# Kernel tuning notes

Hardware: AMD Instinct MI355X
Metric: run time of the kernel (lower is better)

## Reference

```python
import jax, jax.numpy as jnp
import numpy as np

DIM = 256
NH = 8
PD = DIM // 16  # DynamicPosBias pos_dim = (dim//4)//4 = 16
B_ = 256
GH = 16
GW = 16
N = GH * GW
NG = 64


def setup_inputs() -> dict:
    key = jax.random.key(0)
    ks = jax.random.split(key, 24)
    s = 0.05
    inp = {
        "q": jax.random.normal(ks[0], (B_, N, DIM), dtype=jnp.float32),
        "k": jax.random.normal(ks[1], (B_, N, DIM), dtype=jnp.float32),
        "mask": jax.random.normal(ks[2], (NG, N, N), dtype=jnp.float32),
        "q_w": jax.random.normal(ks[3], (DIM, DIM), dtype=jnp.float32) * s,
        "q_b": jnp.zeros((DIM,), jnp.float32),
        "kv_w": jax.random.normal(ks[4], (2 * DIM, DIM), dtype=jnp.float32) * s,
        "kv_b": jnp.zeros((2 * DIM,), jnp.float32),
        "proj_w": jax.random.normal(ks[5], (DIM, DIM), dtype=jnp.float32) * s,
        "proj_b": jnp.zeros((DIM,), jnp.float32),
        "pp_w": jax.random.normal(ks[6], (PD, 2), dtype=jnp.float32) * s,
        "pp_b": jnp.zeros((PD,), jnp.float32),
        "ln1_g": jnp.ones((PD,), jnp.float32),
        "ln1_b": jnp.zeros((PD,), jnp.float32),
        "l1_w": jax.random.normal(ks[7], (PD, PD), dtype=jnp.float32) * s,
        "l1_b": jnp.zeros((PD,), jnp.float32),
        "ln2_g": jnp.ones((PD,), jnp.float32),
        "ln2_b": jnp.zeros((PD,), jnp.float32),
        "l2_w": jax.random.normal(ks[8], (PD, PD), dtype=jnp.float32) * s,
        "l2_b": jnp.zeros((PD,), jnp.float32),
        "ln3_g": jnp.ones((PD,), jnp.float32),
        "ln3_b": jnp.zeros((PD,), jnp.float32),
        "l3_w": jax.random.normal(ks[9], (NH, PD), dtype=jnp.float32) * s,
        "l3_b": jnp.zeros((NH,), jnp.float32),
        "H": GH,
        "W": GW,
    }
    return inp


def _ln(x, g, b):
    m = x.mean(-1, keepdims=True)
    v = ((x - m) ** 2).mean(-1, keepdims=True)
    return (x - m) / jnp.sqrt(v + 1e-5) * g + b


def _pos_bias(H, W, pp_w, pp_b, ln1_g, ln1_b, l1_w, l1_b, ln2_g, ln2_b, l2_w, l2_b, ln3_g, ln3_b, l3_w, l3_b):
    # biases: ((2H-1)*(2W-1), 2) relative offsets
    bh = jnp.arange(1 - H, H, dtype=jnp.float32)
    bw = jnp.arange(1 - W, W, dtype=jnp.float32)
    mg = jnp.stack(jnp.meshgrid(bh, bw, indexing="ij"))  # (2, 2H-1, 2W-1)
    biases = mg.reshape(2, -1).T  # (L, 2)
    # MLP (residual=False): pos3(pos2(pos1(pos_proj(b))))
    x = biases @ pp_w.T + pp_b
    x = _ln(x, ln1_g, ln1_b)
    x = jax.nn.relu(x) @ l1_w.T + l1_b
    x = _ln(x, ln2_g, ln2_b)
    x = jax.nn.relu(x) @ l2_w.T + l2_b
    x = _ln(x, ln3_g, ln3_b)
    pos = jax.nn.relu(x) @ l3_w.T + l3_b  # (L, NH)
    # relative position index (N, N)
    ch = jnp.arange(H)
    cw = jnp.arange(W)
    coords = jnp.stack(jnp.meshgrid(ch, cw, indexing="ij")).reshape(2, -1)  # (2, N)
    rel = coords[:, :, None] - coords[:, None, :]  # (2, N, N)
    rel = rel.transpose(1, 2, 0)
    rel = rel + jnp.array([H - 1, W - 1])
    idx = rel[..., 0] * (2 * W - 1) + rel[..., 1]  # (N, N)
    rpb = pos[idx.reshape(-1)].reshape(H * W, H * W, -1)  # (N, N, NH)
    return rpb.transpose(2, 0, 1)  # (NH, N, N)


def reference(q, k, mask, q_w, q_b, kv_w, kv_b, proj_w, proj_b, pp_w, pp_b,
              ln1_g, ln1_b, l1_w, l1_b, ln2_g, ln2_b, l2_w, l2_b,
              ln3_g, ln3_b, l3_w, l3_b, H, W):
    B, n, C = q.shape
    hd = C // NH
    scale = hd ** -0.5
    qh = (q @ q_w.T + q_b).reshape(B, n, NH, hd).transpose(0, 2, 1, 3)  # (B, NH, N, hd)
    kvh = (k @ kv_w.T + kv_b).reshape(B, n, 2, NH, hd).transpose(2, 0, 3, 1, 4)
    kh, vh = kvh[0], kvh[1]
    attn = jnp.einsum("bhnd,bhmd->bhnm", qh * scale, kh)
    rpb = _pos_bias(H, W, pp_w, pp_b, ln1_g, ln1_b, l1_w, l1_b,
                    ln2_g, ln2_b, l2_w, l2_b, ln3_g, ln3_b, l3_w, l3_b)
    attn = attn + rpb[None]
    nG = mask.shape[0]
    attn = attn.reshape(B // nG, nG, NH, n, n) + mask[None, :, None]
    attn = jax.nn.softmax(attn.reshape(B, NH, n, n), axis=-1)
    x = jnp.einsum("bhnm,bhmd->bhnd", attn, vh).transpose(0, 2, 1, 3).reshape(B, n, C)
    return x @ proj_w.T + proj_b
```

## Files before the change

kernel.cpp:

```cpp
#include <hip/hip_runtime.h>
#include <hip/hip_bf16.h>
#include <cstdint>
#include <cstddef>

typedef __bf16 bf16x8 __attribute__((ext_vector_type(8)));
typedef __bf16 bf16x4 __attribute__((ext_vector_type(4)));
typedef float floatx4 __attribute__((ext_vector_type(4)));
typedef unsigned int uint32x4 __attribute__((ext_vector_type(4)));

__device__ __forceinline__ floatx4 mfma16x16x32(bf16x8 a, bf16x8 b, floatx4 c) {
    return __builtin_amdgcn_mfma_f32_16x16x32_bf16(a, b, c, 0, 0, 0);
}

__device__ __forceinline__ bool flag_is_f32(const void* ones) {
    return *(const unsigned int*)ones == 0x3F800000u;
}
__device__ __forceinline__ float ld1(const void* p, int i, bool f32) {
    return f32 ? ((const float*)p)[i] : (float)((const __bf16*)p)[i];
}
__device__ __forceinline__ bf16x8 ld8(const void* p, size_t i, bool f32) {
    if (f32) {
        const float* f = (const float*)p + i;
        float4 a = *(const float4*)f;
        float4 b = *(const float4*)(f + 4);
        bf16x8 v;
        v[0] = (__bf16)a.x; v[1] = (__bf16)a.y; v[2] = (__bf16)a.z; v[3] = (__bf16)a.w;
        v[4] = (__bf16)b.x; v[5] = (__bf16)b.y; v[6] = (__bf16)b.z; v[7] = (__bf16)b.w;
        return v;
    }
    return *(const bf16x8*)((const __bf16*)p + i);
}
__device__ __forceinline__ unsigned int pk2(float a, float b) {
    __bf16 x = (__bf16)a, y = (__bf16)b;
    unsigned short ux = __builtin_bit_cast(unsigned short, x);
    unsigned short uy = __builtin_bit_cast(unsigned short, y);
    return (unsigned int)ux | ((unsigned int)uy << 16);
}

__device__ __forceinline__ void ln16(float* x, const void* g, const void* b, bool f32) {
    float m = 0.f;
    for (int j = 0; j < 16; ++j) m += x[j];
    m *= (1.f / 16.f);
    float v = 0.f;
    for (int j = 0; j < 16; ++j) { float d = x[j] - m; v += d * d; }
    v *= (1.f / 16.f);
    float inv = rsqrtf(v + 1e-5f);
    for (int j = 0; j < 16; ++j)
        x[j] = (x[j] - m) * inv * ld1(g, j, f32) + ld1(b, j, f32);
}

__global__ void __launch_bounds__(256) k_rpbT(
    const void* __restrict__ pp_w, const void* __restrict__ pp_b,
    const void* __restrict__ g1, const void* __restrict__ b1,
    const void* __restrict__ w1, const void* __restrict__ c1,
    const void* __restrict__ g2, const void* __restrict__ b2,
    const void* __restrict__ w2, const void* __restrict__ c2,
    const void* __restrict__ g3, const void* __restrict__ b3,
    const void* __restrict__ w3, const void* __restrict__ c3,
    __bf16* __restrict__ rpbD)
{
    const bool f32 = flag_is_f32(g1);
    const int bid = blockIdx.x;
    const int ii = bid & 255, h = bid >> 8;
    const int jj = threadIdx.x;
    const int dy = (ii >> 4) - (jj >> 4) + 15;
    const int dx = (ii & 15) - (jj & 15) + 15;
    const float by = (float)(dy - 15), bx = (float)(dx - 15);

    float x[16], y[16];
    for (int o = 0; o < 16; ++o)
        x[o] = by * ld1(pp_w, 2 * o, f32) + bx * ld1(pp_w, 2 * o + 1, f32) + ld1(pp_b, o, f32);
    ln16(x, g1, b1, f32);
    for (int o = 0; o < 16; ++o) {
        float s = ld1(c1, o, f32);
        for (int k = 0; k < 16; ++k) s += fmaxf(x[k], 0.f) * ld1(w1, o * 16 + k, f32);
        y[o] = s;
    }
    ln16(y, g2, b2, f32);
    for (int o = 0; o < 16; ++o) {
        float s = ld1(c2, o, f32);
        for (int k = 0; k < 16; ++k) s += fmaxf(y[k], 0.f) * ld1(w2, o * 16 + k, f32);
        x[o] = s;
    }
    ln16(x, g3, b3, f32);
    float s = ld1(c3, h, f32);
    for (int k = 0; k < 16; ++k) s += fmaxf(x[k], 0.f) * ld1(w3, h * 16 + k, f32);
    rpbD[(size_t)h * 65536 + (size_t)ii * 256 + jj] = (__bf16)s;
}

__global__ void __launch_bounds__(256) k_maskC(const void* __restrict__ mask,
                                               __bf16* __restrict__ maskD,
                                               const void* __restrict__ flag)
{
    const bool f32 = flag_is_f32(flag);
    const size_t i = ((size_t)blockIdx.x * 256 + threadIdx.x) * 8;
    bf16x8 v = ld8(mask, i, f32);
    *(bf16x8*)&maskD[i] = v;
}

template <int MODE>
__global__ void __launch_bounds__(256) k_gemm(
    const void* __restrict__ A, const void* __restrict__ W,
    const void* __restrict__ bias, void* __restrict__ out0,
    __bf16* __restrict__ out1, const void* __restrict__ flag)
{
    __shared__ __bf16 sA[128 * 40];
    __shared__ __bf16 sB[128 * 40];
    const bool in_f32 = flag_is_f32(flag);
    const bool af32 = (MODE == 2) ? false : in_f32;
    const int m0 = blockIdx.x * 128;
    const int n0 = blockIdx.y * 128;
    const int t = threadIdx.x;
    const int w = t >> 6;
    const int lane = t & 63;
    const int lm = lane & 15, q = lane >> 4;

    floatx4 acc[2][8];
    for (int a_ = 0; a_ < 2; ++a_)
        for (int b_ = 0; b_ < 8; ++b_)
            for (int r = 0; r < 4; ++r) acc[a_][b_][r] = 0.f;

    for (int kc = 0; kc < 256; kc += 32) {
        for (int s = 0; s < 2; ++s) {
            int u = t + s * 256;
            int row = u >> 2, seg = u & 3;
            size_t aidx;
            if (MODE == 2) {
                const int m = m0 + row, kk = kc + seg * 8;
                const int b = m >> 8, nn = m & 255, hh = kk >> 5, dd = kk & 31;
                aidx = (((size_t)(b * 8 + hh)) * 256 + nn) * 32 + dd;
            } else {
                aidx = (size_t)(m0 + row) * 256 + kc + seg * 8;
            }
            *(bf16x8*)&sA[row * 40 + seg * 8] = ld8(A, aidx, af32);
            *(bf16x8*)&sB[row * 40 + seg * 8] =
                ld8(W, (size_t)(n0 + row) * 256 + kc + seg * 8, in_f32);
        }
        __syncthreads();
        bf16x8 af[2], bfr[8];
        for (int rt = 0; rt < 2; ++rt)
            af[rt] = *(const bf16x8*)&sA[(w * 32 + rt * 16 + lm) * 40 + q * 8];
        for (int ct = 0; ct < 8; ++ct)
            bfr[ct] = *(const bf16x8*)&sB[(ct * 16 + lm) * 40 + q * 8];
        for (int rt = 0; rt < 2; ++rt)
            for (int ct = 0; ct < 8; ++ct)
                acc[rt][ct] = mfma16x16x32(af[rt], bfr[ct], acc[rt][ct]);
        __syncthreads();
    }

    for (int rt = 0; rt < 2; ++rt) {
        const int rbase = m0 + w * 32 + rt * 16 + q * 4;
        for (int ct = 0; ct < 8; ++ct) {
            const int gc = n0 + ct * 16 + lm;
            const float bv = ld1(bias, gc, in_f32);
            for (int r = 0; r < 4; ++r) {
                const int gr = rbase + r;
                float v = acc[rt][ct][r] + bv;
                if (MODE == 0) {
                    int b = gr >> 8, nn = gr & 255, h = gc >> 5, d = gc & 31;
                    ((__bf16*)out0)[(((size_t)(b * 8 + h)) * 256 + nn) * 32 + d] =
                        (__bf16)(v * 0.17677669529663687f);
                } else if (MODE == 1) {
                    int b = gr >> 8, nn = gr & 255;
                    int f = gc & 255, h = f >> 5, d = f & 31;
                    __bf16* dst = (gc < 256) ? (__bf16*)out0 : out1;
                    dst[(((size_t)(b * 8 + h)) * 256 + nn) * 32 + d] = (__bf16)v;
                } else {
                    if (in_f32) ((float*)out0)[(size_t)gr * 256 + gc] = v;
                    else        ((__bf16*)out0)[(size_t)gr * 256 + gc] = (__bf16)v;
                }
            }
        }
    }
}

__global__ void __launch_bounds__(256, 2) k_attn(
    const __bf16* __restrict__ qs, const __bf16* __restrict__ ks,
    const __bf16* __restrict__ vs, const __bf16* __restrict__ maskD,
    const __bf16* __restrict__ rpbD, __bf16* __restrict__ xb)
{
    __shared__ __bf16 sV[4 * 32 * 266];
    const int bid = blockIdx.x;
    const int x  = bid & 7, rr = bid >> 3;
    const int gl = rr >> 3;
    const int h  = rr & 7;
    const int g  = x + (gl << 3);
    const int t = threadIdx.x, w = t >> 6, lane = t & 63;
    const int lm = lane & 15, q = lane >> 4;
    const __bf16* mD = maskD + (size_t)g * 65536;
    const __bf16* rD = rpbD + (size_t)h * 65536;

    for (int ibat = 0; ibat < 4; ++ibat) {
        const size_t bh = (size_t)((g + (ibat << 6)) * 8 + h);
        const __bf16* vb = vs + bh * 8192;
        __bf16* sVb = sV + ibat * (32 * 266);
        bf16x8 vr[4];
#pragma unroll
        for (int s = 0; s < 4; ++s)
            vr[s] = *(const bf16x8*)&vb[t * 32 + s * 8];
#pragma unroll
        for (int s = 0; s < 4; ++s)
#pragma unroll
            for (int j = 0; j < 8; ++j)
                sVb[(s * 8 + j) * 266 + t] = vr[s][j];
    }
    __syncthreads();

    for (int rt = 0; rt < 4; ++rt) {
        const int row16 = w * 64 + rt * 16;
        const size_t brow = (size_t)(row16 + lm) * 256 + q * 4;
        bf16x4 mv[16], rv[16];
#pragma unroll
        for (int ct = 0; ct < 16; ++ct) {
            mv[ct] = *(const bf16x4*)&mD[brow + ct * 16];
            rv[ct] = *(const bf16x4*)&rD[brow + ct * 16];
        }

        for (int ibat = 0; ibat < 4; ++ibat) {
            const size_t bh = (size_t)((g + (ibat << 6)) * 8 + h);
            const __bf16* qb = qs + bh * 8192;
            const __bf16* kb = ks + bh * 8192;
            const __bf16* sVb = sV + ibat * (32 * 266);
            __bf16* xo = xb + bh * 8192;

            const bf16x8 aq = *(const bf16x8*)&qb[(size_t)(row16 + lm) * 32 + q * 8];

            floatx4 acc[16];
#pragma unroll
            for (int ct = 0; ct < 16; ++ct)
                for (int r = 0; r < 4; ++r) acc[ct][r] = 0.f;
            __builtin_amdgcn_s_setprio(1);
#pragma unroll
            for (int ct = 0; ct < 16; ++ct) {
                const bf16x8 bk = *(const bf16x8*)&kb[(size_t)(ct * 16 + lm) * 32 + q * 8];
                acc[ct] = mfma16x16x32(bk, aq, acc[ct]);
            }
            __builtin_amdgcn_s_setprio(0);
#pragma unroll
            for (int ct = 0; ct < 16; ++ct)
#pragma unroll
                for (int r = 0; r < 4; ++r)
                    acc[ct][r] += (float)mv[ct][r] + (float)rv[ct][r];
            float m = acc[0][0];
#pragma unroll
            for (int ct = 0; ct < 16; ++ct)
                for (int r = 0; r < 4; ++r) m = fmaxf(m, acc[ct][r]);
            m = fmaxf(m, __shfl_xor(m, 16));
            m = fmaxf(m, __shfl_xor(m, 32));
            float ssum = 0.f;
#pragma unroll
            for (int ct = 0; ct < 16; ++ct)
                for (int r = 0; r < 4; ++r) {
                    float p = __expf(acc[ct][r] - m);
                    acc[ct][r] = p;
                    ssum += p;
                }
            ssum += __shfl_xor(ssum, 16);
            ssum += __shfl_xor(ssum, 32);
            const float inv = 1.f / ssum;
            unsigned int pk[16][2];
#pragma unroll
            for (int ct = 0; ct < 16; ++ct) {
                pk[ct][0] = pk2(acc[ct][0], acc[ct][1]);
                pk[ct][1] = pk2(acc[ct][2], acc[ct][3]);
            }
            floatx4 o0, o1;
#pragma unroll
            for (int r = 0; r < 4; ++r) { o0[r] = 0.f; o1[r] = 0.f; }
#pragma unroll
            for (int ct2 = 0; ct2 < 8; ++ct2) {
                uint32x4 dw;
#pragma unroll
                for (int i = 0; i < 4; ++i) {
                    const int srcl = ((q & 1) * 2 + (i >> 1)) * 16 + lm;
                    const int ta = __shfl((int)pk[2 * ct2][i & 1], srcl);
                    const int tb = __shfl((int)pk[2 * ct2 + 1][i & 1], srcl);
                    dw[i] = (q >> 1) ? (unsigned int)tb : (unsigned int)ta;
                }
                const bf16x8 ap = __builtin_bit_cast(bf16x8, dw);
                const bf16x8 bv0 = *(const bf16x8*)&sVb[lm * 266 + ct2 * 32 + q * 8];
                const bf16x8 bv1 = *(const bf16x8*)&sVb[(16 + lm) * 266 + ct2 * 32 + q * 8];
                __builtin_amdgcn_s_setprio(1);
                o0 = mfma16x16x32(ap, bv0, o0);
                o1 = mfma16x16x32(ap, bv1, o1);
                __builtin_amdgcn_s_setprio(0);
            }
#pragma unroll
            for (int r = 0; r < 4; ++r) {
                const float invr = __shfl(inv, (lane & 48) + ((lane >> 4) << 2) + r);
                const size_t row = (size_t)(row16 + q * 4 + r);
                xo[row * 32 + lm]      = (__bf16)(o0[r] * invr);
                xo[row * 32 + 16 + lm] = (__bf16)(o1[r] * invr);
            }
        }
    }
}

extern "C" void kernel_launch(void* const* d_in, const int* in_sizes, int n_in,
                              void* d_out, int out_size, void* d_ws, size_t ws_size,
                              hipStream_t stream)
{
    const void* q      = d_in[0];
    const void* k      = d_in[1];
    const void* mask   = d_in[2];
    const void* q_w    = d_in[3];
    const void* q_b    = d_in[4];
    const void* kv_w   = d_in[5];
    const void* kv_b   = d_in[6];
    const void* proj_w = d_in[7];
    const void* proj_b = d_in[8];
    const void* flag   = d_in[11];

    char* ws = (char*)d_ws;
    __bf16* qs    = (__bf16*)(ws);
    __bf16* ksb   = (__bf16*)(ws + (size_t)33554432);
    __bf16* vsb   = (__bf16*)(ws + (size_t)2 * 33554432);
    __bf16* xbuf  = (__bf16*)(ws + (size_t)3 * 33554432);
    __bf16* maskD = (__bf16*)(ws + (size_t)4 * 33554432);
    __bf16* rpbD  = (__bf16*)(ws + (size_t)4 * 33554432 + 8388608);

    k_rpbT<<<2048, 256, 0, stream>>>(
        d_in[9],  d_in[10], d_in[11], d_in[12], d_in[13], d_in[14],
        d_in[15], d_in[16], d_in[17], d_in[18], d_in[19], d_in[20],
        d_in[21], d_in[22], rpbD);
    k_maskC<<<2048, 256, 0, stream>>>(mask, maskD, flag);
    k_gemm<0><<<dim3(512, 2), 256, 0, stream>>>(q, q_w, q_b, qs, nullptr, flag);
    k_gemm<1><<<dim3(512, 4), 256, 0, stream>>>(k, kv_w, kv_b, ksb, vsb, flag);
    k_attn<<<512, 256, 0, stream>>>(qs, ksb, vsb, maskD, rpbD, xbuf);
    k_gemm<2><<<dim3(512, 2), 256, 0, stream>>>(xbuf, proj_w, proj_b, d_out, nullptr, flag);
}
```

Baseline: 556.3 us.

## Compute pos-bias MLP once per offset and keep full weight tile in LDS for GEMMs

The relative-position MLP now runs once per distinct offset (961 entries) instead of once per (head, i, j) element. A separate gather kernel then expands the results into the per-head bias table. The projection GEMMs are restructured so each block loads the entire 128x256 weight slice into shared memory once. Each wave then streams A rows straight from global memory into registers and loops over several M tiles, which removes the per-K-chunk syncs and repeated weight loads. The cost is a larger LDS footprint that limits occupancy, plus uncoalesced direct A loads.

```diff
diff --git a/kernel.cpp b/kernel.cpp
--- a/kernel.cpp
+++ b/kernel.cpp
@@ -49,7 +49,7 @@
         x[j] = (x[j] - m) * inv * ld1(g, j, f32) + ld1(b, j, f32);
 }
 
-__global__ void __launch_bounds__(256) k_rpbT(
+__global__ void __launch_bounds__(256) k_pos(
     const void* __restrict__ pp_w, const void* __restrict__ pp_b,
     const void* __restrict__ g1, const void* __restrict__ b1,
     const void* __restrict__ w1, const void* __restrict__ c1,
@@ -57,15 +57,12 @@
     const void* __restrict__ w2, const void* __restrict__ c2,
     const void* __restrict__ g3, const void* __restrict__ b3,
     const void* __restrict__ w3, const void* __restrict__ c3,
-    __bf16* __restrict__ rpbD)
+    float* __restrict__ posb)
 {
     const bool f32 = flag_is_f32(g1);
-    const int bid = blockIdx.x;
-    const int ii = bid & 255, h = bid >> 8;
-    const int jj = threadIdx.x;
-    const int dy = (ii >> 4) - (jj >> 4) + 15;
-    const int dx = (ii & 15) - (jj & 15) + 15;
-    const float by = (float)(dy - 15), bx = (float)(dx - 15);
+    const int tid = blockIdx.x * 256 + threadIdx.x;
+    if (tid >= 961) return;
+    const float by = (float)(tid / 31 - 15), bx = (float)(tid % 31 - 15);
 
     float x[16], y[16];
     for (int o = 0; o < 16; ++o)
@@ -83,9 +80,21 @@
         x[o] = s;
     }
     ln16(x, g3, b3, f32);
-    float s = ld1(c3, h, f32);
-    for (int k = 0; k < 16; ++k) s += fmaxf(x[k], 0.f) * ld1(w3, h * 16 + k, f32);
-    rpbD[(size_t)h * 65536 + (size_t)ii * 256 + jj] = (__bf16)s;
+    for (int h = 0; h < 8; ++h) {
+        float s = ld1(c3, h, f32);
+        for (int k = 0; k < 16; ++k) s += fmaxf(x[k], 0.f) * ld1(w3, h * 16 + k, f32);
+        posb[tid * 8 + h] = s;
+    }
+}
+
+__global__ void __launch_bounds__(256) k_rpbX(const float* __restrict__ posb,
+                                              __bf16* __restrict__ rpbD)
+{
+    const int bid = blockIdx.x;
+    const int h = bid >> 8, i = bid & 255, j = threadIdx.x;
+    const int dy = (i >> 4) - (j >> 4) + 15;
+    const int dx = (i & 15) - (j & 15) + 15;
+    rpbD[(size_t)bid * 256 + j] = (__bf16)posb[(dy * 31 + dx) * 8 + h];
 }
 
 __global__ void __launch_bounds__(256) k_maskC(const void* __restrict__ mask,
@@ -99,78 +108,91 @@
 }
 
 template <int MODE>
-__global__ void __launch_bounds__(256) k_gemm(
+__global__ void __launch_bounds__(256, 2) k_gemmS(
     const void* __restrict__ A, const void* __restrict__ W,
     const void* __restrict__ bias, void* __restrict__ out0,
     __bf16* __restrict__ out1, const void* __restrict__ flag)
 {
-    __shared__ __bf16 sA[128 * 40];
-    __shared__ __bf16 sB[128 * 40];
+    constexpr int NT = (MODE == 1) ? 4 : 2;
+    constexpr int SH = (MODE == 1) ? 2 : 1;
+    constexpr int MI = (MODE == 1) ? 4 : 2;
+    __shared__ __bf16 sW[128 * 264];
     const bool in_f32 = flag_is_f32(flag);
     const bool af32 = (MODE == 2) ? false : in_f32;
-    const int m0 = blockIdx.x * 128;
-    const int n0 = blockIdx.y * 128;
-    const int t = threadIdx.x;
-    const int w = t >> 6;
-    const int lane = t & 63;
+    const int bid = blockIdx.x;
+    const int x = bid & 7, rr = bid >> 3;
+    const int n0 = (rr & (NT - 1)) * 128;
+    const int mc = x + ((rr >> SH) << 3);
+    const int m0 = mc * (MI * 128);
+    const int t = threadIdx.x, w = t >> 6, lane = t & 63;
     const int lm = lane & 15, q = lane >> 4;
 
-    floatx4 acc[2][8];
-    for (int a_ = 0; a_ < 2; ++a_)
-        for (int b_ = 0; b_ < 8; ++b_)
-            for (int r = 0; r < 4; ++r) acc[a_][b_][r] = 0.f;
-
-    for (int kc = 0; kc < 256; kc += 32) {
-        for (int s = 0; s < 2; ++s) {
-            int u = t + s * 256;
-            int row = u >> 2, seg = u & 3;
-            size_t aidx;
-            if (MODE == 2) {
-                const int m = m0 + row, kk = kc + seg * 8;
-                const int b = m >> 8, nn = m & 255, hh = kk >> 5, dd = kk & 31;
-                aidx = (((size_t)(b * 8 + hh)) * 256 + nn) * 32 + dd;
-            } else {
-                aidx = (size_t)(m0 + row) * 256 + kc + seg * 8;
-            }
-            *(bf16x8*)&sA[row * 40 + seg * 8] = ld8(A, aidx, af32);
-            *(bf16x8*)&sB[row * 40 + seg * 8] =
-                ld8(W, (size_t)(n0 + row) * 256 + kc + seg * 8, in_f32);
+#pragma unroll
+    for (int s = 0; s < 16; ++s) {
+        const int idx = t + s * 256;
+        const int row = idx >> 5, seg = idx & 31;
+        *(bf16x8*)&sW[row * 264 + seg * 8] =
+            ld8(W, (size_t)(n0 + row) * 256 + seg * 8, in_f32);
+    }
+    __syncthreads();
+
+    for (int it = 0; it < MI; ++it) {
+        const int mrow = m0 + (it * 4 + w) * 32;
+        bf16x8 aq[2][8];
+#pragma unroll
+        for (int half = 0; half < 2; ++half) {
+            const int arow = mrow + half * 16 + lm;
+#pragma unroll
+            for (int kk = 0; kk < 8; ++kk) {
+                size_t aidx;
+                if (MODE == 2) {
+                    const int b = arow >> 8, nn = arow & 255;
+                    aidx = (((size_t)(b * 8 + kk)) * 256 + nn) * 32 + q * 8;
+                } else {
+                    aidx = (size_t)arow * 256 + kk * 32 + q * 8;
+                }
+                aq[half][kk] = ld8(A, aidx, af32);
+            }
         }
-        __syncthreads();
-        bf16x8 af[2], bfr[8];
-        for (int rt = 0; rt < 2; ++rt)
-            af[rt] = *(const bf16x8*)&sA[(w * 32 + rt * 16 + lm) * 40 + q * 8];
-        for (int ct = 0; ct < 8; ++ct)
-            bfr[ct] = *(const bf16x8*)&sB[(ct * 16 + lm) * 40 + q * 8];
-        for (int rt = 0; rt < 2; ++rt)
+        floatx4 acc[2][8];
+#pragma unroll
+        for (int half = 0; half < 2; ++half)
             for (int ct = 0; ct < 8; ++ct)
-                acc[rt][ct] = mfma16x16x32(af[rt], bfr[ct], acc[rt][ct]);
-        __syncthreads();
-    }
-
-    for (int rt = 0; rt < 2; ++rt) {
-        const int rbase = m0 + w * 32 + rt * 16 + q * 4;
-        for (int ct = 0; ct < 8; ++ct) {
-            const int gc = n0 + ct * 16 + lm;
-            const float bv = ld1(bias, gc, in_f32);
-            for (int r = 0; r < 4; ++r) {
-                const int gr = rbase + r;
-                float v = acc[rt][ct][r] + bv;
-                if (MODE == 0) {
-                    int b = gr >> 8, nn = gr & 255, h = gc >> 5, d = gc & 31;
-                    ((__bf16*)out0)[(((size_t)(b * 8 + h)) * 256 + nn) * 32 + d] =
-                        (__bf16)(v * 0.17677669529663687f);
-                } else if (MODE == 1) {
-                    int b = gr >> 8, nn = gr & 255;
-                    int f = gc & 255, h = f >> 5, d = f & 31;
-                    __bf16* dst = (gc < 256) ? (__bf16*)out0 : out1;
-                    dst[(((size_t)(b * 8 + h)) * 256 + nn) * 32 + d] = (__bf16)v;
-                } else {
-                    if (in_f32) ((float*)out0)[(size_t)gr * 256 + gc] = v;
-                    else        ((__bf16*)out0)[(size_t)gr * 256 + gc] = (__bf16)v;
+                for (int r = 0; r < 4; ++r) acc[half][ct][r] = 0.f;
+#pragma unroll
+        for (int kk = 0; kk < 8; ++kk)
+#pragma unroll
+            for (int ct = 0; ct < 8; ++ct) {
+                const bf16x8 bfr =
+                    *(const bf16x8*)&sW[(ct * 16 + lm) * 264 + kk * 32 + q * 8];
+                acc[0][ct] = mfma16x16x32(aq[0][kk], bfr, acc[0][ct]);
+                acc[1][ct] = mfma16x16x32(aq[1][kk], bfr, acc[1][ct]);
+            }
+#pragma unroll
+        for (int half = 0; half < 2; ++half)
+#pragma unroll
+            for (int ct = 0; ct < 8; ++ct) {
+                const int gc = n0 + ct * 16 + lm;
+                const float bv = ld1(bias, gc, in_f32);
+#pragma unroll
+                for (int r = 0; r < 4; ++r) {
+                    const int gr = mrow + half * 16 + q * 4 + r;
+                    float v = acc[half][ct][r] + bv;
+                    if (MODE == 0) {
+                        int b = gr >> 8, nn = gr & 255, h = gc >> 5, d = gc & 31;
+                        ((__bf16*)out0)[(((size_t)(b * 8 + h)) * 256 + nn) * 32 + d] =
+                            (__bf16)(v * 0.17677669529663687f);
+                    } else if (MODE == 1) {
+                        int b = gr >> 8, nn = gr & 255;
+                        int f = gc & 255, h = f >> 5, d = f & 31;
+                        __bf16* dst = (gc < 256) ? (__bf16*)out0 : out1;
+                        dst[(((size_t)(b * 8 + h)) * 256 + nn) * 32 + d] = (__bf16)v;
+                    } else {
+                        if (in_f32) ((float*)out0)[(size_t)gr * 256 + gc] = v;
+                        else        ((__bf16*)out0)[(size_t)gr * 256 + gc] = (__bf16)v;
+                    }
                 }
             }
-        }
     }
 }
 
@@ -318,14 +340,16 @@
     __bf16* xbuf  = (__bf16*)(ws + (size_t)3 * 33554432);
     __bf16* maskD = (__bf16*)(ws + (size_t)4 * 33554432);
     __bf16* rpbD  = (__bf16*)(ws + (size_t)4 * 33554432 + 8388608);
-
-    k_rpbT<<<2048, 256, 0, stream>>>(
+    float*  posb  = (float* )(ws + (size_t)4 * 33554432 + 8388608 + 2097152);
+
+    k_pos<<<4, 256, 0, stream>>>(
         d_in[9],  d_in[10], d_in[11], d_in[12], d_in[13], d_in[14],
         d_in[15], d_in[16], d_in[17], d_in[18], d_in[19], d_in[20],
-        d_in[21], d_in[22], rpbD);
+        d_in[21], d_in[22], posb);
     k_maskC<<<2048, 256, 0, stream>>>(mask, maskD, flag);
-    k_gemm<0><<<dim3(512, 2), 256, 0, stream>>>(q, q_w, q_b, qs, nullptr, flag);
-    k_gemm<1><<<dim3(512, 4), 256, 0, stream>>>(k, kv_w, kv_b, ksb, vsb, flag);
+    k_rpbX<<<2048, 256, 0, stream>>>(posb, rpbD);
+    k_gemmS<0><<<512, 256, 0, stream>>>(q, q_w, q_b, qs, nullptr, flag);
+    k_gemmS<1><<<512, 256, 0, stream>>>(k, kv_w, kv_b, ksb, vsb, flag);
     k_attn<<<512, 256, 0, stream>>>(qs, ksb, vsb, maskD, rpbD, xbuf);
-    k_gemm<2><<<dim3(512, 2), 256, 0, stream>>>(xbuf, proj_w, proj_b, d_out, nullptr, flag);
-}
+    k_gemmS<2><<<512, 256, 0, stream>>>(xbuf, proj_w, proj_b, d_out, nullptr, flag);
+}
```

Result: slower. 670.1 us (+20.5%).
